# Kernel tuning notes

Measured on AMD Instinct MI355X. Metric: run time of the kernel, lower is better.

## Reference

```python
import jax, jax.numpy as jnp
import numpy as np

B, L, S = 128, 400, 30
V, EMB, H, M, OOV = 50000, 128, 512, 512, 30


def setup_inputs():
    ks = jax.random.split(jax.random.key(0), 32)
    rn = lambda k, s, sc=0.05: jax.random.normal(k, s, dtype=jnp.float32) * sc
    return {
        "h": rn(ks[0], (1, B, H), 1.0),
        "word_memory_bank": rn(ks[1], (B, L, M), 1.0),
        "sent_memory_bank": rn(ks[2], (B, S, M), 1.0),
        "src_word_mask": (jax.random.uniform(ks[3], (B, L)) < 0.9).astype(jnp.float32),
        "src_sent_mask": (jax.random.uniform(ks[4], (B, S)) < 0.9).astype(jnp.float32),
        "coverage": jnp.zeros((B, L), jnp.float32),
        "emb_table": rn(ks[5], (V, EMB), 1.0).at[0].set(0.0),  # pad_idx=0 row zeroed
        "gru_w_ih": rn(ks[6], (3 * H, EMB)),
        "gru_w_hh": rn(ks[7], (3 * H, H)),
        "gru_b_ih": rn(ks[8], (3 * H,)),
        "gru_b_hh": rn(ks[9], (3 * H,)),
        "w_mem_proj": rn(ks[10], (H, M)),
        "w_dec_proj_w": rn(ks[11], (H, H)),
        "w_dec_proj_b": rn(ks[12], (H,)),
        "w_v": rn(ks[13], (H,)),
        "w_cov_proj": rn(ks[14], (H,)),
        "s_mem_proj": rn(ks[15], (H, M)),
        "s_dec_proj_w": rn(ks[16], (H, H)),
        "s_dec_proj_b": rn(ks[17], (H,)),
        "s_v": rn(ks[18], (H,)),
        "pgen_w": rn(ks[19], (EMB + H + 2 * M,)),
        "pgen_b": rn(ks[20], (1,)),
        "vd1_w": rn(ks[21], (H, H + 2 * M)),
        "vd1_b": rn(ks[22], (H,)),
        "vd2_w": rn(ks[23], (V, H)),
        "vd2_b": rn(ks[24], (V,)),
        "y": jax.random.randint(ks[25], (B,), 0, V),
        "src_oov": jax.random.randint(ks[26], (B, L), 0, V + OOV),
        "max_num_oovs": OOV,
    }


def _attn_concat(dec, mem, mask, mem_proj, dec_w, dec_b, v, cov=None, cov_proj=None):
    # concat/Bahdanau attention: score = v^T tanh(W_m m + W_d s [+ W_c c])
    feat = jnp.einsum('blm,dm->bld', mem, mem_proj) + (dec @ dec_w.T + dec_b)[:, None, :]
    if cov is not None:
        feat = feat + cov[:, :, None] * cov_proj[None, None, :]
    scores = jnp.einsum('bld,d->bl', jnp.tanh(feat), v)
    attn = jax.nn.softmax(scores, axis=1)
    if mask is not None:  # masked softmax: softmax, mask, renormalize
        attn = attn * mask
        attn = attn / (jnp.sum(attn, axis=1, keepdims=True) + 1e-10)
    ctx = jnp.einsum('bl,blm->bm', attn, mem)
    new_cov = cov + attn if cov is not None else None
    return ctx, attn, new_cov


def _forward(h, word_memory_bank, sent_memory_bank, src_word_mask, src_sent_mask,
             coverage, emb_table, gru_w_ih, gru_w_hh, gru_b_ih, gru_b_hh,
             w_mem_proj, w_dec_proj_w, w_dec_proj_b, w_v, w_cov_proj,
             s_mem_proj, s_dec_proj_w, s_dec_proj_b, s_v,
             pgen_w, pgen_b, vd1_w, vd1_b, vd2_w, vd2_b, y, src_oov, max_num_oovs):
    bsz = src_oov.shape[0]
    y_emb = emb_table[y]  # [B, EMB]
    # single-step GRU (PyTorch gate layout r,z,n)
    gi = y_emb @ gru_w_ih.T + gru_b_ih
    gh = h[-1] @ gru_w_hh.T + gru_b_hh
    ir, iz, inn = jnp.split(gi, 3, axis=1)
    hr, hz, hn = jnp.split(gh, 3, axis=1)
    r = jax.nn.sigmoid(ir + hr)
    z = jax.nn.sigmoid(iz + hz)
    n = jnp.tanh(inn + r * hn)
    h_last = (1.0 - z) * n + z * h[-1]  # [B, H]
    h_next = h_last[None]  # [1, B, H]
    word_ctx, word_attn, word_cov = _attn_concat(
        h_last, word_memory_bank, src_word_mask, w_mem_proj, w_dec_proj_w,
        w_dec_proj_b, w_v, coverage, w_cov_proj)
    sent_ctx, _, _ = _attn_concat(
        h_last, sent_memory_bank, src_sent_mask, s_mem_proj, s_dec_proj_w,
        s_dec_proj_b, s_v)
    context = jnp.concatenate([word_ctx, sent_ctx], axis=1)  # [B, 2M]
    hid = jnp.concatenate([context, h_last], axis=1) @ vd1_w.T + vd1_b
    vocab_dist = jax.nn.softmax(hid @ vd2_w.T + vd2_b, axis=1)  # [B, V]
    pg_in = jnp.concatenate([context, h_last, y_emb], axis=1)
    p_gen = jax.nn.sigmoid(pg_in @ pgen_w + pgen_b)[:, None]  # [B, 1]
    vocab_dist_ = p_gen * vocab_dist
    attn_dist_ = (1.0 - p_gen) * word_attn
    vocab_dist_ = jnp.concatenate(
        [vocab_dist_, jnp.zeros((bsz, max_num_oovs), vocab_dist_.dtype)], axis=1)
    final_dist = vocab_dist_.at[jnp.arange(bsz)[:, None], src_oov].add(attn_dist_)
    return final_dist, h_next, word_ctx, word_attn, p_gen, word_cov


def reference(h, word_memory_bank, sent_memory_bank, src_word_mask, src_sent_mask,
              coverage, emb_table, gru_w_ih, gru_w_hh, gru_b_ih, gru_b_hh,
              w_mem_proj, w_dec_proj_w, w_dec_proj_b, w_v, w_cov_proj,
              s_mem_proj, s_dec_proj_w, s_dec_proj_b, s_v,
              pgen_w, pgen_b, vd1_w, vd1_b, vd2_w, vd2_b, y, src_oov, max_num_oovs):
    return _forward(h, word_memory_bank, sent_memory_bank, src_word_mask,
                    src_sent_mask, coverage, emb_table, gru_w_ih, gru_w_hh,
                    gru_b_ih, gru_b_hh, w_mem_proj, w_dec_proj_w, w_dec_proj_b,
                    w_v, w_cov_proj, s_mem_proj, s_dec_proj_w, s_dec_proj_b,
                    s_v, pgen_w, pgen_b, vd1_w, vd1_b, vd2_w, vd2_b,
                    y, src_oov, max_num_oovs)
```

## Files before the change

kernel.cpp:

```cpp
#include <hip/hip_runtime.h>
#include <hip/hip_bf16.h>
#include <math.h>

#define B 128
#define L 400
#define S 30
#define V 50000
#define EMB 128
#define H 512
#define M 512
#define OOV 30
#define H3 1536
#define VO (V + OOV)

#define O_HN    (B * VO)
#define O_WCTX  (O_HN + B * H)
#define O_WATTN (O_WCTX + B * M)
#define O_PGEN  (O_WATTN + B * L)
#define O_WCOV  (O_PGEN + B)

typedef short bf16x8 __attribute__((ext_vector_type(8)));
typedef float f32x4 __attribute__((ext_vector_type(4)));

__device__ __forceinline__ unsigned pk2(float a, float b) {
    union { __hip_bfloat162 h; unsigned u; } cv;
    cv.h = __float22bfloat162_rn(make_float2(a, b));
    return cv.u;
}

__device__ __forceinline__ float fast_tanh(float x) {
    float e = __expf(2.f * x);
    return 1.f - 2.f * __builtin_amdgcn_rcpf(e + 1.f);
}

__global__ void k_init(const float* __restrict__ bih, const float* __restrict__ bhh,
                       const float* __restrict__ bdpw, const float* __restrict__ bdps,
                       const float* __restrict__ v1b, const float* __restrict__ emb,
                       const int* __restrict__ y,
                       float* gi, float* gh, float* dpw, float* dps, float* hid,
                       float* wscore, float* sscore, float* yemb) {
    int i = blockIdx.x * 256 + threadIdx.x;
    if (i < 196608) { gi[i] = bih[i % 1536]; return; }
    i -= 196608;
    if (i < 196608) { gh[i] = bhh[i % 1536]; return; }
    i -= 196608;
    if (i < 65536) { dpw[i] = bdpw[i & 511]; return; }
    i -= 65536;
    if (i < 65536) { dps[i] = bdps[i & 511]; return; }
    i -= 65536;
    if (i < 65536) { hid[i] = v1b[i & 511]; return; }
    i -= 65536;
    if (i < 51200) { wscore[i] = 0.f; return; }
    i -= 51200;
    if (i < 3840) { sscore[i] = 0.f; return; }
    i -= 3840;
    { int b = i >> 7, e = i & 127; yemb[i] = emb[(size_t)y[b] * EMB + e]; }
}

__global__ void k_cvtw(const float* __restrict__ wih, const float* __restrict__ whh,
                       const float* __restrict__ wdpw, const float* __restrict__ wdps,
                       const float* __restrict__ wmpw, const float* __restrict__ wmps,
                       const float* __restrict__ v1,
                       short* o_ih, short* o_hh, short* o_dpw, short* o_dps,
                       short* o_mpw, short* o_mps, short* o_v1) {
    int bb = blockIdx.x;
    const float* src; short* dst;
    if      (bb < 96)  { src = wih;  dst = o_ih; }
    else if (bb < 480) { src = whh;  dst = o_hh;  bb -= 96; }
    else if (bb < 608) { src = wdpw; dst = o_dpw; bb -= 480; }
    else if (bb < 736) { src = wdps; dst = o_dps; bb -= 608; }
    else if (bb < 864) { src = wmpw; dst = o_mpw; bb -= 736; }
    else if (bb < 992) { src = wmps; dst = o_mps; bb -= 864; }
    else               { src = v1;   dst = o_v1;  bb -= 992; }
    size_t i = (size_t)bb * 2048 + threadIdx.x * 8;
    float4 a = *(const float4*)(src + i);
    float4 c = *(const float4*)(src + i + 4);
    uint4 w;
    w.x = pk2(a.x, a.y); w.y = pk2(a.z, a.w);
    w.z = pk2(c.x, c.y); w.w = pk2(c.z, c.w);
    *(uint4*)(dst + i) = w;
}

__device__ __forceinline__ void stage_a(const float* __restrict__ src, int SK, int rmax,
                                        int t, short dst[128][72]) {
    int col = (t & 7) * 8;
    int r0 = t >> 3;
#pragma unroll
    for (int i = 0; i < 4; ++i) {
        int r = r0 + i * 32;
        int rr = r < rmax ? r : rmax;
        const float* p = src + (size_t)rr * SK + col;
        float4 a = *(const float4*)p;
        float4 c = *(const float4*)(p + 4);
        uint4 w;
        w.x = pk2(a.x, a.y); w.y = pk2(a.z, a.w);
        w.z = pk2(c.x, c.y); w.w = pk2(c.z, c.w);
        *(uint4*)&dst[r][col] = w;
    }
}

__device__ __forceinline__ void stage_b128bf(const short* __restrict__ src, int K,
                                             int t, short dst[128][72]) {
    int col = (t & 7) * 8;
    int r0 = t >> 3;
#pragma unroll
    for (int i = 0; i < 4; ++i) {
        int r = r0 + i * 32;
        *(bf16x8*)&dst[r][col] = *(const bf16x8*)(src + (size_t)r * K + col);
    }
}

__device__ __forceinline__ void stage_b256bf(const short* __restrict__ src, int K,
                                             int t, short dst[256][72]) {
    int col = (t & 7) * 8;
    int r0 = t >> 3;
#pragma unroll
    for (int i = 0; i < 8; ++i) {
        int r = r0 + i * 32;
        *(bf16x8*)&dst[r][col] = *(const bf16x8*)(src + (size_t)r * K + col);
    }
}

__global__ __launch_bounds__(256, 2) void k_mmsk(
        const float* __restrict__ A0, const short* __restrict__ B0, float* __restrict__ C0,
        int K0, int NT0, int KB0,
        const float* __restrict__ A1, const short* __restrict__ B1, float* __restrict__ C1,
        int K1, int NT1, int KB1) {
    __shared__ short As[128][72];
    __shared__ short Bs[128][72];
    int t = threadIdx.x, lane = t & 63, wv = t >> 6;
    int wr = wv >> 1, wc = wv & 1;
    int l15 = lane & 15, l4 = lane >> 4;

    int bb = blockIdx.x;
    const float* A; const short* Bb; float* C; int K, NT, KB;
    if (bb < NT0 * KB0) { A = A0; Bb = B0; C = C0; K = K0; NT = NT0; KB = KB0; }
    else { bb -= NT0 * KB0; A = A1; Bb = B1; C = C1; K = K1; NT = NT1; KB = KB1; }
    int nIdx = bb % NT, kIdx = bb / NT;
    int ldc = NT * 128;
    int nBase = nIdx * 128;
    int KC = K / KB;
    int kLo = kIdx * KC, kHi = kLo + KC;

    f32x4 acc[4][4] = {};
    for (int kc = kLo; kc < kHi; kc += 64) {
        stage_a(A + kc, K, 127, t, As);
        stage_b128bf(Bb + (size_t)nBase * K + kc, K, t, Bs);
        __syncthreads();
#pragma unroll
        for (int kk = 0; kk < 2; ++kk) {
            bf16x8 af[4], bq[4];
#pragma unroll
            for (int i = 0; i < 4; ++i)
                af[i] = *(const bf16x8*)&As[wr * 64 + i * 16 + l15][kk * 32 + l4 * 8];
#pragma unroll
            for (int j = 0; j < 4; ++j)
                bq[j] = *(const bf16x8*)&Bs[wc * 64 + j * 16 + l15][kk * 32 + l4 * 8];
#pragma unroll
            for (int i = 0; i < 4; ++i)
#pragma unroll
                for (int j = 0; j < 4; ++j)
                    acc[i][j] = __builtin_amdgcn_mfma_f32_16x16x32_bf16(
                        af[i], bq[j], acc[i][j], 0, 0, 0);
        }
        __syncthreads();
    }
#pragma unroll
    for (int i = 0; i < 4; ++i)
#pragma unroll
        for (int r = 0; r < 4; ++r) {
            int row = wr * 64 + i * 16 + l4 * 4 + r;
#pragma unroll
            for (int j = 0; j < 4; ++j) {
                int n = nBase + wc * 64 + j * 16 + l15;
                atomicAdd(&C[(size_t)row * ldc + n], acc[i][j][r]);
            }
        }
}

__global__ __launch_bounds__(256, 2) void k_mm128(
        const float* __restrict__ Ap, const float* __restrict__ Bf,
        const float* __restrict__ bias, float* __restrict__ C, int K, int ldc, int Nlim) {
    __shared__ short As[128][72];
    __shared__ short Bs[128][72];
    int t = threadIdx.x, lane = t & 63, wv = t >> 6;
    int wr = wv >> 1, wc = wv & 1;
    int l15 = lane & 15, l4 = lane >> 4;
    int nBase = blockIdx.x * 128;
    int brmax = Nlim - 1 - nBase; if (brmax > 127) brmax = 127;

    f32x4 acc[4][4] = {};
    for (int kc = 0; kc < K; kc += 64) {
        stage_a(Ap + kc, K, 127, t, As);
        stage_a(Bf + (size_t)nBase * K + kc, K, brmax, t, Bs);
        __syncthreads();
#pragma unroll
        for (int kk = 0; kk < 2; ++kk) {
            bf16x8 af[4], bq[4];
#pragma unroll
            for (int i = 0; i < 4; ++i)
                af[i] = *(const bf16x8*)&As[wr * 64 + i * 16 + l15][kk * 32 + l4 * 8];
#pragma unroll
            for (int j = 0; j < 4; ++j)
                bq[j] = *(const bf16x8*)&Bs[wc * 64 + j * 16 + l15][kk * 32 + l4 * 8];
#pragma unroll
            for (int i = 0; i < 4; ++i)
#pragma unroll
                for (int j = 0; j < 4; ++j)
                    acc[i][j] = __builtin_amdgcn_mfma_f32_16x16x32_bf16(
                        af[i], bq[j], acc[i][j], 0, 0, 0);
        }
        __syncthreads();
    }
#pragma unroll
    for (int i = 0; i < 4; ++i)
#pragma unroll
        for (int r = 0; r < 4; ++r) {
            int row = wr * 64 + i * 16 + l4 * 4 + r;
#pragma unroll
            for (int j = 0; j < 4; ++j) {
                int n = nBase + wc * 64 + j * 16 + l15;
                if (n < Nlim) C[(size_t)row * ldc + n] = acc[i][j][r] + bias[n];
            }
        }
}

__global__ __launch_bounds__(256, 2) void k_feat2(
        const float* __restrict__ wmb, const short* __restrict__ wbmpw,
        const float* __restrict__ dpw, const float* __restrict__ cov,
        const float* __restrict__ covp, const float* __restrict__ vw,
        float* __restrict__ wscore,
        const float* __restrict__ smb, const short* __restrict__ wbmps,
        const float* __restrict__ dps, const float* __restrict__ vs,
        float* __restrict__ sscore) {
    __shared__ short As[128][72];
    __shared__ short Bs[256][72];
    int t = threadIdx.x, lane = t & 63, wv = t >> 6;
    int wr = wv >> 1, wc = wv & 1;
    int l15 = lane & 15, l4 = lane >> 4;

    bool word = blockIdx.y < 400;
    const float* Ap; const short* Bbf; const float* dproj; const float* vvec; float* outp;
    int rowBase;
    if (word) { Ap = wmb; Bbf = wbmpw; dproj = dpw; vvec = vw; outp = wscore; rowBase = blockIdx.y * 128; }
    else      { Ap = smb; Bbf = wbmps; dproj = dps; vvec = vs; outp = sscore; rowBase = (blockIdx.y - 400) * 128; }
    int nBase = blockIdx.x * 256;
    const float* Asrc = Ap + (size_t)rowBase * 512;
    const short* Bsrc = Bbf + (size_t)nBase * 512;

    f32x4 acc[4][8] = {};
    for (int kc = 0; kc < 512; kc += 64) {
        stage_a(Asrc + kc, 512, 127, t, As);
        stage_b256bf(Bsrc + kc, 512, t, Bs);
        __syncthreads();
#pragma unroll
        for (int kk = 0; kk < 2; ++kk) {
            bf16x8 af[4], bq[8];
#pragma unroll
            for (int i = 0; i < 4; ++i)
                af[i] = *(const bf16x8*)&As[wr * 64 + i * 16 + l15][kk * 32 + l4 * 8];
#pragma unroll
            for (int j = 0; j < 8; ++j)
                bq[j] = *(const bf16x8*)&Bs[wc * 128 + j * 16 + l15][kk * 32 + l4 * 8];
#pragma unroll
            for (int i = 0; i < 4; ++i)
#pragma unroll
                for (int j = 0; j < 8; ++j)
                    acc[i][j] = __builtin_amdgcn_mfma_f32_16x16x32_bf16(
                        af[i], bq[j], acc[i][j], 0, 0, 0);
        }
        __syncthreads();
    }
    int dB = nBase + wc * 128;
    float vv[8], cp[8], dp0[8], dp1[8];
    int b0 = word ? rowBase / 400 : 0;
    int b1 = word ? (rowBase + 127) / 400 : 0;
#pragma unroll
    for (int j = 0; j < 8; ++j) {
        int d = dB + j * 16 + l15;
        vv[j] = vvec[d];
        cp[j] = word ? covp[d] : 0.f;
        if (word) { dp0[j] = dproj[b0 * H + d]; dp1[j] = dproj[b1 * H + d]; }
    }
#pragma unroll
    for (int i = 0; i < 4; ++i) {
#pragma unroll
        for (int r = 0; r < 4; ++r) {
            int row = rowBase + wr * 64 + i * 16 + l4 * 4 + r;
            int b = word ? (row / 400) : (row / 30);
            float cv = word ? cov[row] : 0.f;
            bool use0 = (b == b0);
            float s = 0.f;
#pragma unroll
            for (int j = 0; j < 8; ++j) {
                float dpv = word ? (use0 ? dp0[j] : dp1[j])
                                 : dproj[b * H + dB + j * 16 + l15];
                float f = acc[i][j][r] + dpv + cv * cp[j];
                s += vv[j] * fast_tanh(f);
            }
            s += __shfl_xor(s, 8, 16);
            s += __shfl_xor(s, 4, 16);
            s += __shfl_xor(s, 2, 16);
            s += __shfl_xor(s, 1, 16);
            if (l15 == 0) atomicAdd(&outp[row], s);
        }
    }
}

__global__ void k_gates(const float* __restrict__ gi, const float* __restrict__ gh,
                        const float* __restrict__ h, float* __restrict__ hnext) {
    int i = blockIdx.x * 256 + threadIdx.x;
    int b = i >> 9, k = i & 511;
    float ir = gi[b * H3 + k], iz = gi[b * H3 + H + k], inn = gi[b * H3 + 2 * H + k];
    float hr = gh[b * H3 + k], hz = gh[b * H3 + H + k], hn = gh[b * H3 + 2 * H + k];
    float r = 1.f / (1.f + __expf(-(ir + hr)));
    float z = 1.f / (1.f + __expf(-(iz + hz)));
    float n = fast_tanh(inn + r * hn);
    hnext[i] = (1.f - z) * n + z * h[i];
}

__global__ __launch_bounds__(256) void k_smax_sent(
        const float* __restrict__ wscore, const float* __restrict__ wmask,
        const float* __restrict__ cov, float* __restrict__ wattn, float* __restrict__ wcov,
        const float* __restrict__ sscore, const float* __restrict__ smask,
        const float* __restrict__ smb, float* __restrict__ sctx) {
    __shared__ float sc[L];
    __shared__ float red[4];
    int t = threadIdx.x;
    if (blockIdx.x < B) {
        int b = blockIdx.x;
        float mx = -1e30f;
        for (int l = t; l < L; l += 256) { float s = wscore[b * L + l]; sc[l] = s; mx = fmaxf(mx, s); }
        for (int off = 32; off; off >>= 1) mx = fmaxf(mx, __shfl_xor(mx, off));
        if ((t & 63) == 0) red[t >> 6] = mx;
        __syncthreads();
        mx = fmaxf(fmaxf(red[0], red[1]), fmaxf(red[2], red[3]));
        __syncthreads();
        float sm = 0.f;
        for (int l = t; l < L; l += 256) { float e = __expf(sc[l] - mx); sc[l] = e; sm += e; }
        for (int off = 32; off; off >>= 1) sm += __shfl_xor(sm, off);
        if ((t & 63) == 0) red[t >> 6] = sm;
        __syncthreads();
        float Z = red[0] + red[1] + red[2] + red[3];
        __syncthreads();
        float sm2 = 0.f;
        for (int l = t; l < L; l += 256) {
            float a = (sc[l] / Z) * wmask[b * L + l];
            sc[l] = a; sm2 += a;
        }
        for (int off = 32; off; off >>= 1) sm2 += __shfl_xor(sm2, off);
        if ((t & 63) == 0) red[t >> 6] = sm2;
        __syncthreads();
        float Zm = red[0] + red[1] + red[2] + red[3] + 1e-10f;
        for (int l = t; l < L; l += 256) {
            float a = sc[l] / Zm;
            wattn[b * L + l] = a;
            wcov[b * L + l] = cov[b * L + l] + a;
        }
    } else {
        int b = blockIdx.x - B;
        float* sa = sc; float* sa2 = sc + 32; float* smk = sc + 64;
        if (t < S) { sa[t] = sscore[b * S + t]; smk[t] = smask[b * S + t]; }
        __syncthreads();
        if (t < S) {
            float mx = -1e30f;
            for (int l = 0; l < S; ++l) mx = fmaxf(mx, sa[l]);
            float Z = 0.f, Zm = 0.f;
            for (int l = 0; l < S; ++l) { float e = __expf(sa[l] - mx); Z += e; Zm += e * smk[l]; }
            float e = __expf(sa[t] - mx);
            float a = (e / Z) * smk[t];
            sa2[t] = a / (Zm / Z + 1e-10f);
        }
        __syncthreads();
        float a0 = 0.f, a1 = 0.f;
        for (int l = 0; l < S; ++l) {
            const float* r = smb + ((size_t)b * S + l) * M;
            float a = sa2[l];
            a0 += a * r[t]; a1 += a * r[t + 256];
        }
        sctx[b * M + t] = a0; sctx[b * M + t + 256] = a1;
    }
}

__global__ __launch_bounds__(256) void k_ctx_part(
        const float* __restrict__ attn, const float* __restrict__ memb,
        float* __restrict__ ctxp) {
    __shared__ float sa[100];
    int b = blockIdx.y, ch = blockIdx.x, t = threadIdx.x;
    int l0 = ch * 100;
    if (t < 100) sa[t] = attn[b * L + l0 + t];
    __syncthreads();
    float ax = 0.f, ay = 0.f;
    const float* base = memb + ((size_t)b * L + l0) * M + t * 2;
#pragma unroll 4
    for (int l = 0; l < 100; ++l) {
        float2 m2 = *(const float2*)(base + (size_t)l * M);
        float a = sa[l];
        ax += a * m2.x; ay += a * m2.y;
    }
    float* o = ctxp + ((size_t)(ch * B + b)) * M + t * 2;
    o[0] = ax; o[1] = ay;
}

__global__ void k_ctx_red(const float* __restrict__ ctxp, float* __restrict__ wctx,
                          float* __restrict__ cat) {
    int j = blockIdx.x * 256 + threadIdx.x;
    float v = ctxp[j] + ctxp[B * M + j] + ctxp[2 * B * M + j] + ctxp[3 * B * M + j];
    wctx[j] = v;
    int b = j >> 9, c = j & 511;
    cat[b * H3 + c] = v;
}

__global__ void k_catpgen(const float* __restrict__ sctx, const float* __restrict__ hlast,
                          const float* __restrict__ wctx, const float* __restrict__ yemb,
                          const float* __restrict__ pw, const float* __restrict__ pb,
                          float* __restrict__ cat, float* __restrict__ pg) {
    int bb = blockIdx.x, t = threadIdx.x;
    if (bb < 512) {
        int i = bb * 256 + t;
        int b = i >> 10, c = i & 1023;
        cat[b * H3 + 512 + c] = (c < 512) ? sctx[b * 512 + c] : hlast[b * 512 + c - 512];
    } else {
        int b = bb - 512;
        if (t < 64) {
            float s = 0.f;
            for (int i = t; i < EMB + H + 2 * M; i += 64) {
                float x = (i < 512) ? wctx[b * H + i]
                        : (i < 1024) ? sctx[b * H + i - 512]
                        : (i < 1536) ? hlast[b * H + i - 1024]
                                     : yemb[b * EMB + i - 1536];
                s += x * pw[i];
            }
            for (int off = 32; off; off >>= 1) s += __shfl_xor(s, off);
            if (t == 0) pg[b] = 1.f / (1.f + __expf(-(s + pb[0])));
        }
    }
}

__global__ __launch_bounds__(256) void k_vpart(
        const float* __restrict__ logits, float* __restrict__ pm, float* __restrict__ ps) {
    __shared__ float wm[4], wsv[4];
    int b = blockIdx.y, c = blockIdx.x, t = threadIdx.x;
    const float4* row = (const float4*)(logits + (size_t)b * V) + c * 1250;
    float m = -3e38f, s = 0.f;
    for (int i = t; i < 1250; i += 256) {
        float4 x = row[i];
        float m4 = fmaxf(fmaxf(x.x, x.y), fmaxf(x.z, x.w));
        if (m4 > m) { s *= __expf(m - m4); m = m4; }
        s += __expf(x.x - m) + __expf(x.y - m) + __expf(x.z - m) + __expf(x.w - m);
    }
    for (int off = 32; off; off >>= 1) {
        float mo = __shfl_xor(m, off), so = __shfl_xor(s, off);
        float mn = fmaxf(m, mo);
        s = s * __expf(m - mn) + so * __expf(mo - mn);
        m = mn;
    }
    if ((t & 63) == 0) { wm[t >> 6] = m; wsv[t >> 6] = s; }
    __syncthreads();
    if (t == 0) {
        float M2 = fmaxf(fmaxf(wm[0], wm[1]), fmaxf(wm[2], wm[3]));
        float S2 = wsv[0] * __expf(wm[0] - M2) + wsv[1] * __expf(wm[1] - M2) +
                   wsv[2] * __expf(wm[2] - M2) + wsv[3] * __expf(wm[3] - M2);
        pm[b * 10 + c] = M2; ps[b * 10 + c] = S2;
    }
}

__global__ __launch_bounds__(256) void k_vwrite(
        const float* __restrict__ logits, const float* __restrict__ pm,
        const float* __restrict__ ps, const float* __restrict__ pgen,
        float* __restrict__ fd) {
    int b = blockIdx.y, t = threadIdx.x;
    float M2 = -3e38f;
#pragma unroll
    for (int c = 0; c < 10; ++c) M2 = fmaxf(M2, pm[b * 10 + c]);
    float S2 = 0.f;
#pragma unroll
    for (int c = 0; c < 10; ++c) S2 += ps[b * 10 + c] * __expf(pm[b * 10 + c] - M2);
    float inv = pgen[b] / S2;
    int col0 = blockIdx.x * 2048 + t * 8;
    float* outb = fd + (size_t)b * VO;
    if (col0 + 8 <= V) {
        const float4* lp = (const float4*)(logits + (size_t)b * V + col0);
        float4 x = lp[0], z = lp[1];
        *(float2*)(outb + col0)     = make_float2(inv * __expf(x.x - M2), inv * __expf(x.y - M2));
        *(float2*)(outb + col0 + 2) = make_float2(inv * __expf(x.z - M2), inv * __expf(x.w - M2));
        *(float2*)(outb + col0 + 4) = make_float2(inv * __expf(z.x - M2), inv * __expf(z.y - M2));
        *(float2*)(outb + col0 + 6) = make_float2(inv * __expf(z.z - M2), inv * __expf(z.w - M2));
    } else {
#pragma unroll
        for (int k = 0; k < 8; k += 2) {
            int c = col0 + k;
            if (c + 2 <= VO) {
                float2 o;
                o.x = (c < V)     ? inv * __expf(logits[(size_t)b * V + c] - M2) : 0.f;
                o.y = (c + 1 < V) ? inv * __expf(logits[(size_t)b * V + c + 1] - M2) : 0.f;
                *(float2*)(outb + c) = o;
            }
        }
    }
}

__global__ void k_scatter(const int* __restrict__ oov, const float* __restrict__ wattn,
                          const float* __restrict__ pgen, float* __restrict__ fd) {
    int i = blockIdx.x * 256 + threadIdx.x;
    int b = i / L;
    float w = (1.f - pgen[b]) * wattn[i];
    atomicAdd(&fd[(size_t)b * VO + oov[i]], w);
}

extern "C" void kernel_launch(void* const* d_in, const int* in_sizes, int n_in,
                              void* d_out, int out_size, void* d_ws, size_t ws_size,
                              hipStream_t stream) {
    const float* h     = (const float*)d_in[0];
    const float* wmb   = (const float*)d_in[1];
    const float* smb   = (const float*)d_in[2];
    const float* wmask = (const float*)d_in[3];
    const float* smask = (const float*)d_in[4];
    const float* cov   = (const float*)d_in[5];
    const float* emb   = (const float*)d_in[6];
    const float* Wih   = (const float*)d_in[7];
    const float* Whh   = (const float*)d_in[8];
    const float* bih   = (const float*)d_in[9];
    const float* bhh   = (const float*)d_in[10];
    const float* Wmpw  = (const float*)d_in[11];
    const float* Wdpw  = (const float*)d_in[12];
    const float* bdpw  = (const float*)d_in[13];
    const float* vw    = (const float*)d_in[14];
    const float* covp  = (const float*)d_in[15];
    const float* Wmps  = (const float*)d_in[16];
    const float* Wdps  = (const float*)d_in[17];
    const float* bdps  = (const float*)d_in[18];
    const float* vs    = (const float*)d_in[19];
    const float* pw    = (const float*)d_in[20];
    const float* pb    = (const float*)d_in[21];
    const float* vd1w  = (const float*)d_in[22];
    const float* vd1b  = (const float*)d_in[23];
    const float* vd2w  = (const float*)d_in[24];
    const float* vd2b  = (const float*)d_in[25];
    const int*   y     = (const int*)d_in[26];
    const int*   oov   = (const int*)d_in[27];

    float* out   = (float*)d_out;
    float* fd    = out;
    float* hnext = out + O_HN;
    float* wctx  = out + O_WCTX;
    float* wattn = out + O_WATTN;
    float* pgen  = out + O_PGEN;
    float* wcov  = out + O_WCOV;

    float* ws     = (float*)d_ws;
    float* yemb   = ws;
    float* gi     = yemb + B * EMB;
    float* gh     = gi + B * H3;
    float* dpw    = gh + B * H3;
    float* dps    = dpw + B * H;
    float* wscore = dps + B * H;
    float* sscore = wscore + B * L;
    float* sctx   = sscore + B * S;
    float* hid    = sctx + B * M;
    float* logits = hid + B * H;
    float* cat    = gi;
    float* ctxp   = logits;
    short* wb     = (short*)(logits + (size_t)B * V);
    short* wb_ih  = wb;
    short* wb_hh  = wb_ih + H3 * EMB;
    short* wb_dpw = wb_hh + H3 * H;
    short* wb_dps = wb_dpw + H * H;
    short* wb_mpw = wb_dps + H * H;
    short* wb_mps = wb_mpw + H * M;
    short* wb_v1  = wb_mps + H * M;
    float* pm     = (float*)(wb_v1 + H * H3);
    float* psum   = pm + B * 10;

    k_init<<<2583, 256, 0, stream>>>(bih, bhh, bdpw, bdps, vd1b, emb, y,
                                     gi, gh, dpw, dps, hid, wscore, sscore, yemb);
    k_cvtw<<<1376, 256, 0, stream>>>(Wih, Whh, Wdpw, Wdps, Wmpw, Wmps, vd1w,
                                     wb_ih, wb_hh, wb_dpw, wb_dps, wb_mpw, wb_mps, wb_v1);
    k_mmsk<<<36, 256, 0, stream>>>(yemb, wb_ih, gi, 128, 12, 1,
                                   h, wb_hh, gh, 512, 12, 2);
    k_gates<<<256, 256, 0, stream>>>(gi, gh, h, hnext);
    k_mmsk<<<16, 256, 0, stream>>>(hnext, wb_dpw, dpw, 512, 4, 2,
                                   hnext, wb_dps, dps, 512, 4, 2);
    k_feat2<<<dim3(2, 430), 256, 0, stream>>>(wmb, wb_mpw, dpw, cov, covp, vw, wscore,
                                              smb, wb_mps, dps, vs, sscore);
    k_smax_sent<<<2 * B, 256, 0, stream>>>(wscore, wmask, cov, wattn, wcov,
                                           sscore, smask, smb, sctx);
    k_ctx_part<<<dim3(4, B), 256, 0, stream>>>(wattn, wmb, ctxp);
    k_ctx_red<<<(B * M) / 256, 256, 0, stream>>>(ctxp, wctx, cat);
    k_catpgen<<<512 + B, 256, 0, stream>>>(sctx, hnext, wctx, yemb, pw, pb, cat, pgen);
    k_mmsk<<<24, 256, 0, stream>>>(cat, wb_v1, hid, 1536, 4, 6,
                                   nullptr, nullptr, nullptr, 64, 1, 0);
    k_mm128<<<(V + 127) / 128, 256, 0, stream>>>(hid, vd2w, vd2b, logits, H, V, V);
    k_vpart<<<dim3(10, B), 256, 0, stream>>>(logits, pm, psum);
    k_vwrite<<<dim3(25, B), 256, 0, stream>>>(logits, pm, psum, pgen, fd);
    k_scatter<<<200, 256, 0, stream>>>(oov, wattn, pgen, fd);
}
```

Before: 236.3 us.

## Merge setup kernels, shrink feat tile to 128 columns, fuse ctx reduce into cat

Merges the init and weight-conversion kernels into a single launch, and likewise folds the context reduction into the concat/p_gen kernel, with p_gen recomputing the word context from the partial sums. This removes two kernel launches and their inter-kernel gaps. The attention feature kernel now uses a 128x128 tile instead of 128x256, which halves shared memory and accumulator registers, doubles the grid, and raises the occupancy hint to 4 blocks per CU. The cost is that the fp32 memory-bank A tile is loaded and converted twice as often, and the decoder projection is read per element instead of from preloaded registers.

```diff
diff --git a/kernel.cpp b/kernel.cpp
--- a/kernel.cpp
+++ b/kernel.cpp
@@ -33,37 +33,39 @@
     return 1.f - 2.f * __builtin_amdgcn_rcpf(e + 1.f);
 }
 
-__global__ void k_init(const float* __restrict__ bih, const float* __restrict__ bhh,
-                       const float* __restrict__ bdpw, const float* __restrict__ bdps,
-                       const float* __restrict__ v1b, const float* __restrict__ emb,
-                       const int* __restrict__ y,
-                       float* gi, float* gh, float* dpw, float* dps, float* hid,
-                       float* wscore, float* sscore, float* yemb) {
-    int i = blockIdx.x * 256 + threadIdx.x;
-    if (i < 196608) { gi[i] = bih[i % 1536]; return; }
-    i -= 196608;
-    if (i < 196608) { gh[i] = bhh[i % 1536]; return; }
-    i -= 196608;
-    if (i < 65536) { dpw[i] = bdpw[i & 511]; return; }
-    i -= 65536;
-    if (i < 65536) { dps[i] = bdps[i & 511]; return; }
-    i -= 65536;
-    if (i < 65536) { hid[i] = v1b[i & 511]; return; }
-    i -= 65536;
-    if (i < 51200) { wscore[i] = 0.f; return; }
-    i -= 51200;
-    if (i < 3840) { sscore[i] = 0.f; return; }
-    i -= 3840;
-    { int b = i >> 7, e = i & 127; yemb[i] = emb[(size_t)y[b] * EMB + e]; }
-}
-
-__global__ void k_cvtw(const float* __restrict__ wih, const float* __restrict__ whh,
-                       const float* __restrict__ wdpw, const float* __restrict__ wdps,
-                       const float* __restrict__ wmpw, const float* __restrict__ wmps,
-                       const float* __restrict__ v1,
-                       short* o_ih, short* o_hh, short* o_dpw, short* o_dps,
-                       short* o_mpw, short* o_mps, short* o_v1) {
+__global__ void k_setup(const float* __restrict__ bih, const float* __restrict__ bhh,
+                        const float* __restrict__ bdpw, const float* __restrict__ bdps,
+                        const float* __restrict__ v1b, const float* __restrict__ emb,
+                        const int* __restrict__ y,
+                        float* gi, float* gh, float* dpw, float* dps, float* hid,
+                        float* wscore, float* sscore, float* yemb,
+                        const float* __restrict__ wih, const float* __restrict__ whh,
+                        const float* __restrict__ wdpw, const float* __restrict__ wdps,
+                        const float* __restrict__ wmpw, const float* __restrict__ wmps,
+                        const float* __restrict__ v1,
+                        short* o_ih, short* o_hh, short* o_dpw, short* o_dps,
+                        short* o_mpw, short* o_mps, short* o_v1) {
     int bb = blockIdx.x;
+    if (bb < 2583) {
+        int i = bb * 256 + threadIdx.x;
+        if (i < 196608) { gi[i] = bih[i % 1536]; return; }
+        i -= 196608;
+        if (i < 196608) { gh[i] = bhh[i % 1536]; return; }
+        i -= 196608;
+        if (i < 65536) { dpw[i] = bdpw[i & 511]; return; }
+        i -= 65536;
+        if (i < 65536) { dps[i] = bdps[i & 511]; return; }
+        i -= 65536;
+        if (i < 65536) { hid[i] = v1b[i & 511]; return; }
+        i -= 65536;
+        if (i < 51200) { wscore[i] = 0.f; return; }
+        i -= 51200;
+        if (i < 3840) { sscore[i] = 0.f; return; }
+        i -= 3840;
+        if (i < 16384) { int b = i >> 7, e = i & 127; yemb[i] = emb[(size_t)y[b] * EMB + e]; }
+        return;
+    }
+    bb -= 2583;
     const float* src; short* dst;
     if      (bb < 96)  { src = wih;  dst = o_ih; }
     else if (bb < 480) { src = whh;  dst = o_hh;  bb -= 96; }
@@ -110,17 +112,6 @@
     }
 }
 
-__device__ __forceinline__ void stage_b256bf(const short* __restrict__ src, int K,
-                                             int t, short dst[256][72]) {
-    int col = (t & 7) * 8;
-    int r0 = t >> 3;
-#pragma unroll
-    for (int i = 0; i < 8; ++i) {
-        int r = r0 + i * 32;
-        *(bf16x8*)&dst[r][col] = *(const bf16x8*)(src + (size_t)r * K + col);
-    }
-}
-
 __global__ __launch_bounds__(256, 2) void k_mmsk(
         const float* __restrict__ A0, const short* __restrict__ B0, float* __restrict__ C0,
         int K0, int NT0, int KB0,
@@ -225,7 +216,7 @@
         }
 }
 
-__global__ __launch_bounds__(256, 2) void k_feat2(
+__global__ __launch_bounds__(256, 4) void k_feat(
         const float* __restrict__ wmb, const short* __restrict__ wbmpw,
         const float* __restrict__ dpw, const float* __restrict__ cov,
         const float* __restrict__ covp, const float* __restrict__ vw,
@@ -234,7 +225,7 @@
         const float* __restrict__ dps, const float* __restrict__ vs,
         float* __restrict__ sscore) {
     __shared__ short As[128][72];
-    __shared__ short Bs[256][72];
+    __shared__ short Bs[128][72];
     int t = threadIdx.x, lane = t & 63, wv = t >> 6;
     int wr = wv >> 1, wc = wv & 1;
     int l15 = lane & 15, l4 = lane >> 4;
@@ -244,43 +235,40 @@
     int rowBase;
     if (word) { Ap = wmb; Bbf = wbmpw; dproj = dpw; vvec = vw; outp = wscore; rowBase = blockIdx.y * 128; }
     else      { Ap = smb; Bbf = wbmps; dproj = dps; vvec = vs; outp = sscore; rowBase = (blockIdx.y - 400) * 128; }
-    int nBase = blockIdx.x * 256;
+    int nBase = blockIdx.x * 128;
     const float* Asrc = Ap + (size_t)rowBase * 512;
     const short* Bsrc = Bbf + (size_t)nBase * 512;
 
-    f32x4 acc[4][8] = {};
+    f32x4 acc[4][4] = {};
     for (int kc = 0; kc < 512; kc += 64) {
         stage_a(Asrc + kc, 512, 127, t, As);
-        stage_b256bf(Bsrc + kc, 512, t, Bs);
+        stage_b128bf(Bsrc + kc, 512, t, Bs);
         __syncthreads();
 #pragma unroll
         for (int kk = 0; kk < 2; ++kk) {
-            bf16x8 af[4], bq[8];
+            bf16x8 af[4], bq[4];
 #pragma unroll
             for (int i = 0; i < 4; ++i)
                 af[i] = *(const bf16x8*)&As[wr * 64 + i * 16 + l15][kk * 32 + l4 * 8];
 #pragma unroll
-            for (int j = 0; j < 8; ++j)
-                bq[j] = *(const bf16x8*)&Bs[wc * 128 + j * 16 + l15][kk * 32 + l4 * 8];
+            for (int j = 0; j < 4; ++j)
+                bq[j] = *(const bf16x8*)&Bs[wc * 64 + j * 16 + l15][kk * 32 + l4 * 8];
 #pragma unroll
             for (int i = 0; i < 4; ++i)
 #pragma unroll
-                for (int j = 0; j < 8; ++j)
+                for (int j = 0; j < 4; ++j)
                     acc[i][j] = __builtin_amdgcn_mfma_f32_16x16x32_bf16(
                         af[i], bq[j], acc[i][j], 0, 0, 0);
         }
         __syncthreads();
     }
-    int dB = nBase + wc * 128;
-    float vv[8], cp[8], dp0[8], dp1[8];
-    int b0 = word ? rowBase / 400 : 0;
-    int b1 = word ? (rowBase + 127) / 400 : 0;
-#pragma unroll
-    for (int j = 0; j < 8; ++j) {
+    int dB = nBase + wc * 64;
+    float vv[4], cp[4];
+#pragma unroll
+    for (int j = 0; j < 4; ++j) {
         int d = dB + j * 16 + l15;
         vv[j] = vvec[d];
         cp[j] = word ? covp[d] : 0.f;
-        if (word) { dp0[j] = dproj[b0 * H + d]; dp1[j] = dproj[b1 * H + d]; }
     }
 #pragma unroll
     for (int i = 0; i < 4; ++i) {
@@ -289,12 +277,10 @@
             int row = rowBase + wr * 64 + i * 16 + l4 * 4 + r;
             int b = word ? (row / 400) : (row / 30);
             float cv = word ? cov[row] : 0.f;
-            bool use0 = (b == b0);
             float s = 0.f;
 #pragma unroll
-            for (int j = 0; j < 8; ++j) {
-                float dpv = word ? (use0 ? dp0[j] : dp1[j])
-                                 : dproj[b * H + dB + j * 16 + l15];
+            for (int j = 0; j < 4; ++j) {
+                float dpv = dproj[b * H + dB + j * 16 + l15];
                 float f = acc[i][j][r] + dpv + cv * cp[j];
                 s += vv[j] * fast_tanh(f);
             }
@@ -402,33 +388,34 @@
     o[0] = ax; o[1] = ay;
 }
 
-__global__ void k_ctx_red(const float* __restrict__ ctxp, float* __restrict__ wctx,
-                          float* __restrict__ cat) {
-    int j = blockIdx.x * 256 + threadIdx.x;
-    float v = ctxp[j] + ctxp[B * M + j] + ctxp[2 * B * M + j] + ctxp[3 * B * M + j];
-    wctx[j] = v;
-    int b = j >> 9, c = j & 511;
-    cat[b * H3 + c] = v;
-}
-
-__global__ void k_catpgen(const float* __restrict__ sctx, const float* __restrict__ hlast,
-                          const float* __restrict__ wctx, const float* __restrict__ yemb,
-                          const float* __restrict__ pw, const float* __restrict__ pb,
-                          float* __restrict__ cat, float* __restrict__ pg) {
+__global__ void k_ctxcat(const float* __restrict__ ctxp, const float* __restrict__ sctx,
+                         const float* __restrict__ hnext, const float* __restrict__ yemb,
+                         const float* __restrict__ pw, const float* __restrict__ pb,
+                         float* __restrict__ wctx, float* __restrict__ cat,
+                         float* __restrict__ pg) {
     int bb = blockIdx.x, t = threadIdx.x;
-    if (bb < 512) {
-        int i = bb * 256 + t;
+    if (bb < 256) {
+        int j = bb * 256 + t;
+        float v = ctxp[j] + ctxp[B * M + j] + ctxp[2 * B * M + j] + ctxp[3 * B * M + j];
+        wctx[j] = v;
+        int b = j >> 9, c = j & 511;
+        cat[b * H3 + c] = v;
+    } else if (bb < 768) {
+        int i = (bb - 256) * 256 + t;
         int b = i >> 10, c = i & 1023;
-        cat[b * H3 + 512 + c] = (c < 512) ? sctx[b * 512 + c] : hlast[b * 512 + c - 512];
+        cat[b * H3 + 512 + c] = (c < 512) ? sctx[b * 512 + c] : hnext[b * 512 + c - 512];
     } else {
-        int b = bb - 512;
+        int b = bb - 768;
         if (t < 64) {
             float s = 0.f;
             for (int i = t; i < EMB + H + 2 * M; i += 64) {
-                float x = (i < 512) ? wctx[b * H + i]
-                        : (i < 1024) ? sctx[b * H + i - 512]
-                        : (i < 1536) ? hlast[b * H + i - 1024]
-                                     : yemb[b * EMB + i - 1536];
+                float x;
+                if (i < 512) {
+                    int j = b * 512 + i;
+                    x = ctxp[j] + ctxp[B * M + j] + ctxp[2 * B * M + j] + ctxp[3 * B * M + j];
+                } else if (i < 1024) x = sctx[b * 512 + i - 512];
+                else if (i < 1536)   x = hnext[b * 512 + i - 1024];
+                else                 x = yemb[b * EMB + i - 1536];
                 s += x * pw[i];
             }
             for (int off = 32; off; off >>= 1) s += __shfl_xor(s, off);
@@ -572,22 +559,22 @@
     float* pm     = (float*)(wb_v1 + H * H3);
     float* psum   = pm + B * 10;
 
-    k_init<<<2583, 256, 0, stream>>>(bih, bhh, bdpw, bdps, vd1b, emb, y,
-                                     gi, gh, dpw, dps, hid, wscore, sscore, yemb);
-    k_cvtw<<<1376, 256, 0, stream>>>(Wih, Whh, Wdpw, Wdps, Wmpw, Wmps, vd1w,
-                                     wb_ih, wb_hh, wb_dpw, wb_dps, wb_mpw, wb_mps, wb_v1);
+    k_setup<<<2583 + 1376, 256, 0, stream>>>(bih, bhh, bdpw, bdps, vd1b, emb, y,
+                                             gi, gh, dpw, dps, hid, wscore, sscore, yemb,
+                                             Wih, Whh, Wdpw, Wdps, Wmpw, Wmps, vd1w,
+                                             wb_ih, wb_hh, wb_dpw, wb_dps, wb_mpw, wb_mps, wb_v1);
     k_mmsk<<<36, 256, 0, stream>>>(yemb, wb_ih, gi, 128, 12, 1,
                                    h, wb_hh, gh, 512, 12, 2);
     k_gates<<<256, 256, 0, stream>>>(gi, gh, h, hnext);
     k_mmsk<<<16, 256, 0, stream>>>(hnext, wb_dpw, dpw, 512, 4, 2,
                                    hnext, wb_dps, dps, 512, 4, 2);
-    k_feat2<<<dim3(2, 430), 256, 0, stream>>>(wmb, wb_mpw, dpw, cov, covp, vw, wscore,
-                                              smb, wb_mps, dps, vs, sscore);
+    k_feat<<<dim3(4, 430), 256, 0, stream>>>(wmb, wb_mpw, dpw, cov, covp, vw, wscore,
+                                             smb, wb_mps, dps, vs, sscore);
     k_smax_sent<<<2 * B, 256, 0, stream>>>(wscore, wmask, cov, wattn, wcov,
                                            sscore, smask, smb, sctx);
     k_ctx_part<<<dim3(4, B), 256, 0, stream>>>(wattn, wmb, ctxp);
-    k_ctx_red<<<(B * M) / 256, 256, 0, stream>>>(ctxp, wctx, cat);
-    k_catpgen<<<512 + B, 256, 0, stream>>>(sctx, hnext, wctx, yemb, pw, pb, cat, pgen);
+    k_ctxcat<<<768 + B, 256, 0, stream>>>(ctxp, sctx, hnext, yemb, pw, pb,
+                                          wctx, cat, pgen);
     k_mmsk<<<24, 256, 0, stream>>>(cat, wb_v1, hid, 1536, 4, 6,
                                    nullptr, nullptr, nullptr, 64, 1, 0);
     k_mm128<<<(V + 127) / 128, 256, 0, stream>>>(hid, vd2w, vd2b, logits, H, V, V);
```

New measurement: 265.0 us. +12.1%, slower.
